# Kernel optimization log

Hardware: AMD Instinct MI355X
Metric: run time of the kernel (lower is better)

Reference implementation:

```python
import jax, jax.numpy as jnp
import numpy as np

B, L, NUM_AA, E, H = 128, 2048, 20, 16, 128

def _mlp(x, W1, b1, W2, b2, W3, b3):
    h = jax.nn.relu(x @ W1 + b1)
    h = jax.nn.relu(h @ W2 + b2)
    return h @ W3 + b3

def _mlp_params(key, in_dim):
    k1, k2, k3 = jax.random.split(key, 3)
    W1 = jax.random.normal(k1, (in_dim, H), jnp.float32) / np.sqrt(in_dim)
    W2 = jax.random.normal(k2, (H, H), jnp.float32) / np.sqrt(H)
    W3 = jax.random.normal(k3, (H, 1), jnp.float32) / np.sqrt(H)
    return W1, jnp.zeros((H,), jnp.float32), W2, jnp.zeros((H,), jnp.float32), W3, jnp.zeros((1,), jnp.float32)

def setup_inputs() -> dict:
    key = jax.random.key(0)
    kR, ks, ke, kl, kt, kp = jax.random.split(key, 6)
    inp = {
        'R': jax.random.normal(kR, (B, L, 3), jnp.float32) * 3.8,  # ~CA-CA scale
        'seq': jax.random.randint(ks, (B, L), 0, NUM_AA),
        'emb': jax.random.normal(ke, (NUM_AA, E), jnp.float32),
    }
    for pref, k, d in (('fl', kl, 1 + 2 * E), ('ft', kt, 1 + 3 * E), ('fp', kp, 2 + 4 * E)):
        W1, b1, W2, b2, W3, b3 = _mlp_params(k, d)
        inp.update({f'{pref}_W1': W1, f'{pref}_b1': b1, f'{pref}_W2': W2, f'{pref}_b2': b2, f'{pref}_W3': W3, f'{pref}_b3': b3})
    return inp

def _energy(R, e, fl, ft, fp):
    d = R[:, 1:, :] - R[:, :-1, :]                      # [B,L-1,3] bond vectors
    lengths = jnp.linalg.norm(d, axis=-1)               # [B,L-1]
    x_l = jnp.concatenate([lengths[..., None], e[:, :-1, :], e[:, 1:, :]], axis=-1)
    E_l = _mlp(x_l, *fl)[..., 0].sum(axis=1)
    # bond angles at atom i+1 between (R[i]-R[i+1]) and (R[i+2]-R[i+1])
    u, v = -d[:, :-1, :], d[:, 1:, :]                   # [B,L-2,3]
    cos_t = jnp.sum(u * v, axis=-1) / (jnp.linalg.norm(u, axis=-1) * jnp.linalg.norm(v, axis=-1))
    theta_in = jnp.clip(cos_t, -1.0, 1.0)               # use_cos_theta=True -> cos(arccos(clip))
    x_t = jnp.concatenate([theta_in[..., None], e[:, :-2, :], e[:, 1:-1, :], e[:, 2:, :]], axis=-1)
    E_t = _mlp(x_t, *ft)[..., 0].sum(axis=1)
    # torsions over quadruples
    b1, b2, b3 = d[:, :-2, :], d[:, 1:-1, :], d[:, 2:, :]
    n1 = jnp.cross(b1, b2)
    n2 = jnp.cross(b2, b3)
    b2u = b2 / jnp.linalg.norm(b2, axis=-1, keepdims=True)
    m1 = jnp.cross(n1, b2u)
    phi = jnp.arctan2(jnp.sum(m1 * n2, axis=-1), jnp.sum(n1 * n2, axis=-1))  # [B,L-3]
    sc = jnp.stack([jnp.sin(phi), jnp.cos(phi)], axis=-1)                    # [B,L-3,2]
    x_p = jnp.concatenate([sc, e[:, :-3, :], e[:, 1:-2, :], e[:, 2:-1, :], e[:, 3:, :]], axis=-1)
    E_p = _mlp(x_p, *fp)[..., 0].sum(axis=1)
    return E_l + E_t + E_p

def reference(R, seq, emb,
              fl_W1, fl_b1, fl_W2, fl_b2, fl_W3, fl_b3,
              ft_W1, ft_b1, ft_W2, ft_b2, ft_W3, ft_b3,
              fp_W1, fp_b1, fp_W2, fp_b2, fp_W3, fp_b3):
    e = emb[seq]                                        # [B,L,E]
    return _energy(R, e,
                   (fl_W1, fl_b1, fl_W2, fl_b2, fl_W3, fl_b3),
                   (ft_W1, ft_b1, ft_W2, ft_b2, ft_W3, ft_b3),
                   (fp_W1, fp_b1, fp_W2, fp_b2, fp_W3, fp_b3))
```

## Files before the change

kernel.cpp:

```cpp
#include <hip/hip_runtime.h>


typedef short bf16x8 __attribute__((ext_vector_type(8)));
typedef float f32x4  __attribute__((ext_vector_type(4)));

constexpr int Lc  = 2048;
constexpr int SHs = 136;

union FragU { uint4 u; bf16x8 v; };

__device__ __forceinline__ unsigned short f2bf(float f) {
    union { float f; unsigned u; } v; v.f = f;
    unsigned u = v.u;
    u = u + 0x7FFFu + ((u >> 16) & 1u);
    return (unsigned short)(u >> 16);
}

__device__ __forceinline__ unsigned pkbf(float a, float b) {
    unsigned ua = __float_as_uint(a) + 0x8000u;
    unsigned ub = __float_as_uint(b) + 0x8000u;
    return __builtin_amdgcn_perm(ub, ua, 0x07060302u);
}

__global__ __launch_bounds__(256)
void prep_kernel(const float* __restrict__ W1_0, const float* __restrict__ b1_0,
                 const float* __restrict__ W1_1, const float* __restrict__ b1_1,
                 const float* __restrict__ W1_2, const float* __restrict__ b1_2,
                 const float* __restrict__ W2_0, const float* __restrict__ W2_1,
                 const float* __restrict__ W2_2,
                 const float* __restrict__ emb, char* __restrict__ ws,
                 float* __restrict__ out)
{
    const int tid = blockIdx.x * 256 + threadIdx.x;
    const int np  = gridDim.x * 256;
    if (blockIdx.x == 0 && threadIdx.x < 128) out[threadIdx.x] = 0.0f;

    unsigned short* d2 = (unsigned short*)ws;
    for (int o = tid; o < 3 * 16384; o += np) {
        int t = o >> 14, r = o & 16383, col = r >> 7, k = r & 127;
        const float* W2 = (t == 0) ? W2_0 : (t == 1) ? W2_1 : W2_2;
        d2[o] = f2bf(W2[k * 128 + col]);
    }
    unsigned short* d1 = (unsigned short*)(ws + 98304);
    for (int o = tid; o < 3 * 12288; o += np) {
        int t = o / 12288, r = o - t * 12288, hid = r / 96, k = r - hid * 96;
        const int NE16 = (t == 0) ? 32 : (t == 1) ? 48 : 64;
        const int NG   = (t == 2) ? 2 : 1;
        const float* W1 = (t == 0) ? W1_0 : (t == 1) ? W1_1 : W1_2;
        const float* b1 = (t == 0) ? b1_0 : (t == 1) ? b1_1 : b1_2;
        float v = 0.0f;
        if (k >= 16) {
            int j = k - 16;
            if (j < NE16) v = W1[(NG + j) * 128 + hid];
        } else if (k == 4) v = b1[hid];
        else if (t == 0 && k == 0) v = W1_0[hid];
        else if (t == 1 && k == 1) v = W1_1[hid];
        else if (t == 2 && k == 2) v = W1_2[hid];
        else if (t == 2 && k == 3) v = W1_2[128 + hid];
        d1[o] = f2bf(v);
    }
    unsigned short* eb = (unsigned short*)(ws + 172032);
    for (int i = tid; i < 320; i += np) eb[i] = f2bf(emb[i]);
}

struct SMem {
    unsigned short H1s[64 * SHs];
    float  Rbuf[393];
    uint2  geomh[128];
    int    seqb[132];
    unsigned short ebuf[320];
    float  part[4];
};

template<int TYPE, int H>
__device__ __forceinline__ void half_pass(
    SMem& sm, const char* __restrict__ ws,
    const float* __restrict__ b2, const float* __restrict__ w3,
    int i0, int wv, int q, int c, f32x4& p4)
{
    constexpr int NEMB  = (TYPE == 0) ? 2 : (TYPE == 1) ? 3 : 4;
    constexpr int KS    = (TYPE == 2) ? 3 : 2;
    constexpr int ROWSB = Lc - 1 - TYPE;

    const unsigned short* w1t = (const unsigned short*)(ws + 98304 + TYPE * 24576);
    const unsigned short* w2t = (const unsigned short*)(ws + TYPE * 32768);

    FragU A1[2][3];
#pragma unroll
    for (int mt = 0; mt < 2; ++mt)
#pragma unroll
        for (int ks = 0; ks < KS; ++ks)
            A1[mt][ks].u = *(const uint4*)&w1t[(wv * 32 + mt * 16 + c) * 96 + ks * 32 + q * 8];

    f32x4 acc1[2][4];
#pragma unroll
    for (int mt = 0; mt < 2; ++mt)
#pragma unroll
        for (int nt = 0; nt < 4; ++nt)
            acc1[mt][nt] = (f32x4){0.f, 0.f, 0.f, 0.f};

#pragma unroll
    for (int ks = 0; ks < KS; ++ks) {
        const int k0 = ks * 32 + q * 8;
        const int j = (k0 - 16) >> 4, off = (k0 - 16) & 15;
#pragma unroll
        for (int nt = 0; nt < 4; ++nt) {
            const int m = H * 64 + nt * 16 + c;
            FragU bb;
            if (ks == 0 && q == 0) {
                uint2 g = sm.geomh[m];
                bb.u = make_uint4(g.x, g.y, 0x00003F80u, 0u);
            } else if (k0 >= 16 && j < NEMB) {
                bb.u = *(const uint4*)&sm.ebuf[sm.seqb[m + j] * 16 + off];
            } else {
                bb.u = make_uint4(0u, 0u, 0u, 0u);
            }
            acc1[0][nt] = __builtin_amdgcn_mfma_f32_16x16x32_bf16(A1[0][ks].v, bb.v, acc1[0][nt], 0, 0, 0);
            acc1[1][nt] = __builtin_amdgcn_mfma_f32_16x16x32_bf16(A1[1][ks].v, bb.v, acc1[1][nt], 0, 0, 0);
        }
    }

    const f32x4 z4 = (f32x4){0.f, 0.f, 0.f, 0.f};
#pragma unroll
    for (int mt = 0; mt < 2; ++mt)
#pragma unroll
        for (int nt = 0; nt < 4; ++nt) {
            f32x4 v = __builtin_elementwise_max(acc1[mt][nt], z4);
            uint2 pk;
            pk.x = pkbf(v[0], v[1]);
            pk.y = pkbf(v[2], v[3]);
            *(uint2*)&sm.H1s[(nt * 16 + c) * SHs + wv * 32 + mt * 16 + q * 4] = pk;
        }

    FragU B2[2][4];
#pragma unroll
    for (int nt = 0; nt < 2; ++nt)
#pragma unroll
        for (int ks = 0; ks < 4; ++ks)
            B2[nt][ks].u = *(const uint4*)&w2t[(wv * 32 + nt * 16 + c) * 128 + ks * 32 + q * 8];
    float b2v[2], w3v[2];
#pragma unroll
    for (int nt = 0; nt < 2; ++nt) {
        int col2 = wv * 32 + nt * 16 + c;
        b2v[nt] = b2[col2]; w3v[nt] = w3[col2];
    }
    __syncthreads();

    f32x4 acc2[4][2];
#pragma unroll
    for (int mt = 0; mt < 4; ++mt)
#pragma unroll
        for (int nt = 0; nt < 2; ++nt)
            acc2[mt][nt] = (f32x4){0.f, 0.f, 0.f, 0.f};
#pragma unroll
    for (int ks = 0; ks < 4; ++ks)
#pragma unroll
        for (int mt = 0; mt < 4; ++mt) {
            bf16x8 aa = *(const bf16x8*)&sm.H1s[(mt * 16 + c) * SHs + ks * 32 + q * 8];
            acc2[mt][0] = __builtin_amdgcn_mfma_f32_16x16x32_bf16(aa, B2[0][ks].v, acc2[mt][0], 0, 0, 0);
            acc2[mt][1] = __builtin_amdgcn_mfma_f32_16x16x32_bf16(aa, B2[1][ks].v, acc2[mt][1], 0, 0, 0);
        }

#pragma unroll
    for (int mt = 0; mt < 4; ++mt) {
        int mbase = H * 64 + mt * 16 + q * 4;
        if (i0 + mbase + 3 < ROWSB) {
#pragma unroll
            for (int nt = 0; nt < 2; ++nt) {
                f32x4 v = acc2[mt][nt] + b2v[nt];
                v = __builtin_elementwise_max(v, z4);
                p4 += v * w3v[nt];
            }
        } else {
#pragma unroll
            for (int rg = 0; rg < 4; ++rg)
                if (i0 + mbase + rg < ROWSB) {
                    p4[rg] += fmaxf(acc2[mt][0][rg] + b2v[0], 0.f) * w3v[0];
                    p4[rg] += fmaxf(acc2[mt][1][rg] + b2v[1], 0.f) * w3v[1];
                }
        }
    }
    __syncthreads();
}

__global__ __launch_bounds__(256, 4)
void energy_kernel(const float* __restrict__ R, const int* __restrict__ seq,
                   const char* __restrict__ ws,
                   const float* b2_0, const float* b2_1, const float* b2_2,
                   const float* w3_0, const float* w3_1, const float* w3_2,
                   const float* b3_0, const float* b3_1, const float* b3_2,
                   float* __restrict__ out)
{
    __shared__ SMem sm;
    const int tid = threadIdx.x;
    const int b   = blockIdx.y;
    const int i0  = blockIdx.x * 128;
    const int lane = tid & 63, wv = tid >> 6;
    const int q = lane >> 4, c = lane & 15;

    for (int t = tid; t < 393; t += 256) {
        int lr = t / 3, comp = t - lr * 3;
        int row = min(i0 + lr, Lc - 1);
        sm.Rbuf[t] = R[((size_t)b * Lc + row) * 3 + comp];
    }
    for (int t = tid; t < 131; t += 256)
        sm.seqb[t] = seq[b * Lc + min(i0 + t, Lc - 1)];
    {
        const uint4* se = (const uint4*)(ws + 172032);
        for (int t = tid; t < 40; t += 256) ((uint4*)sm.ebuf)[t] = se[t];
    }
    __syncthreads();

    if (tid < 128) {
        const float* p0 = &sm.Rbuf[tid * 3];
        float ax = p0[3] - p0[0], ay = p0[4] - p0[1], az = p0[5] - p0[2];
        float bx = p0[6] - p0[3], by = p0[7] - p0[4], bz = p0[8] - p0[5];
        float cx = p0[9] - p0[6], cy = p0[10] - p0[7], cz = p0[11] - p0[8];
        float na2 = ax * ax + ay * ay + az * az;
        float len = sqrtf(na2);
        float nb2 = bx * bx + by * by + bz * bz;
        float duv = -(ax * bx + ay * by + az * bz);
        float cost = fminf(fmaxf(duv / sqrtf(na2 * nb2), -1.0f), 1.0f);
        float n1x = ay * bz - az * by, n1y = az * bx - ax * bz, n1z = ax * by - ay * bx;
        float n2x = by * cz - bz * cy, n2y = bz * cx - bx * cz, n2z = bx * cy - by * cx;
        float binv = 1.0f / sqrtf(nb2);
        float ux = bx * binv, uy = by * binv, uz = bz * binv;
        float m1x = n1y * uz - n1z * uy, m1y = n1z * ux - n1x * uz, m1z = n1x * uy - n1y * ux;
        float yv = m1x * n2x + m1y * n2y + m1z * n2z;
        float xv = n1x * n2x + n1y * n2y + n1z * n2z;
        float inv = 1.0f / sqrtf(xv * xv + yv * yv);
        sm.geomh[tid] = make_uint2(pkbf(len, cost), pkbf(yv * inv, xv * inv));
    }
    __syncthreads();

    f32x4 p4 = (f32x4){0.f, 0.f, 0.f, 0.f};
    half_pass<0, 0>(sm, ws, b2_0, w3_0, i0, wv, q, c, p4);
    half_pass<0, 1>(sm, ws, b2_0, w3_0, i0, wv, q, c, p4);
    half_pass<1, 0>(sm, ws, b2_1, w3_1, i0, wv, q, c, p4);
    half_pass<1, 1>(sm, ws, b2_1, w3_1, i0, wv, q, c, p4);
    half_pass<2, 0>(sm, ws, b2_2, w3_2, i0, wv, q, c, p4);
    half_pass<2, 1>(sm, ws, b2_2, w3_2, i0, wv, q, c, p4);

    float p = p4[0] + p4[1] + p4[2] + p4[3];
#pragma unroll
    for (int off = 32; off > 0; off >>= 1)
        p += __shfl_down(p, off);
    if (lane == 0) sm.part[wv] = p;
    __syncthreads();
    if (tid == 0) {
        float tot = sm.part[0] + sm.part[1] + sm.part[2] + sm.part[3];
        tot += b3_0[0] * (float)min(Lc - 1 - i0, 128);
        tot += b3_1[0] * (float)min(Lc - 2 - i0, 128);
        tot += b3_2[0] * (float)min(Lc - 3 - i0, 128);
        atomicAdd(&out[b], tot);
    }
}

extern "C" void kernel_launch(void* const* d_in, const int* in_sizes, int n_in,
                              void* d_out, int out_size, void* d_ws, size_t ws_size,
                              hipStream_t stream) {
    const float* R   = (const float*)d_in[0];
    const int*   seq = (const int*)d_in[1];
    const float* emb = (const float*)d_in[2];
    float* out = (float*)d_out;
    char*  ws  = (char*)d_ws;

    prep_kernel<<<dim3(96), dim3(256), 0, stream>>>(
        (const float*)d_in[3],  (const float*)d_in[4],
        (const float*)d_in[9],  (const float*)d_in[10],
        (const float*)d_in[15], (const float*)d_in[16],
        (const float*)d_in[5],  (const float*)d_in[11], (const float*)d_in[17],
        emb, ws, out);

    dim3 grid(16, 128), block(256);
    energy_kernel<<<grid, block, 0, stream>>>(
        R, seq, ws,
        (const float*)d_in[6],  (const float*)d_in[12], (const float*)d_in[18],
        (const float*)d_in[7],  (const float*)d_in[13], (const float*)d_in[19],
        (const float*)d_in[8],  (const float*)d_in[14], (const float*)d_in[20],
        out);
}
```

Baseline: 165.7 us.

## Give each wave its own 32 rows to drop block-wide barriers in MLP passes

Rewrites the per-block MLP work split so each wave owns 32 sequence rows and computes all 128 hidden units for them, instead of splitting hidden columns across waves. Each wave gets a private H1 staging buffer, and the geometry features for its rows are computed by the same wave, so all the __syncthreads between layers and passes are removed. In exchange every wave now streams the full W1 and W2 weight tiles from global/L2 for every row tile, and holds more accumulators, so occupancy is lowered to 3 blocks per CU.

Result: slower. 245.2 us (+48.0%).

```diff
diff --git a/kernel.cpp b/kernel.cpp
--- a/kernel.cpp
+++ b/kernel.cpp
@@ -64,7 +64,7 @@
 }
 
 struct SMem {
-    unsigned short H1s[64 * SHs];
+    unsigned short H1s[4][32 * SHs];
     float  Rbuf[393];
     uint2  geomh[128];
     int    seqb[132];
@@ -72,8 +72,8 @@
     float  part[4];
 };
 
-template<int TYPE, int H>
-__device__ __forceinline__ void half_pass(
+template<int TYPE>
+__device__ __forceinline__ void type_pass(
     SMem& sm, const char* __restrict__ ws,
     const float* __restrict__ b2, const float* __restrict__ w3,
     int i0, int wv, int q, int c, f32x4& p4)
@@ -84,89 +84,86 @@
 
     const unsigned short* w1t = (const unsigned short*)(ws + 98304 + TYPE * 24576);
     const unsigned short* w2t = (const unsigned short*)(ws + TYPE * 32768);
-
-    FragU A1[2][3];
-#pragma unroll
-    for (int mt = 0; mt < 2; ++mt)
-#pragma unroll
-        for (int ks = 0; ks < KS; ++ks)
-            A1[mt][ks].u = *(const uint4*)&w1t[(wv * 32 + mt * 16 + c) * 96 + ks * 32 + q * 8];
-
-    f32x4 acc1[2][4];
-#pragma unroll
-    for (int mt = 0; mt < 2; ++mt)
-#pragma unroll
-        for (int nt = 0; nt < 4; ++nt)
+    unsigned short* H1w = sm.H1s[wv];
+
+    f32x4 acc1[8][2];
+#pragma unroll
+    for (int mt = 0; mt < 8; ++mt)
+#pragma unroll
+        for (int nt = 0; nt < 2; ++nt)
             acc1[mt][nt] = (f32x4){0.f, 0.f, 0.f, 0.f};
 
 #pragma unroll
     for (int ks = 0; ks < KS; ++ks) {
         const int k0 = ks * 32 + q * 8;
         const int j = (k0 - 16) >> 4, off = (k0 - 16) & 15;
-#pragma unroll
-        for (int nt = 0; nt < 4; ++nt) {
-            const int m = H * 64 + nt * 16 + c;
-            FragU bb;
+        FragU bb[2];
+#pragma unroll
+        for (int nt = 0; nt < 2; ++nt) {
+            const int m = wv * 32 + nt * 16 + c;
             if (ks == 0 && q == 0) {
                 uint2 g = sm.geomh[m];
-                bb.u = make_uint4(g.x, g.y, 0x00003F80u, 0u);
+                bb[nt].u = make_uint4(g.x, g.y, 0x00003F80u, 0u);
             } else if (k0 >= 16 && j < NEMB) {
-                bb.u = *(const uint4*)&sm.ebuf[sm.seqb[m + j] * 16 + off];
+                bb[nt].u = *(const uint4*)&sm.ebuf[sm.seqb[m + j] * 16 + off];
             } else {
-                bb.u = make_uint4(0u, 0u, 0u, 0u);
+                bb[nt].u = make_uint4(0u, 0u, 0u, 0u);
             }
-            acc1[0][nt] = __builtin_amdgcn_mfma_f32_16x16x32_bf16(A1[0][ks].v, bb.v, acc1[0][nt], 0, 0, 0);
-            acc1[1][nt] = __builtin_amdgcn_mfma_f32_16x16x32_bf16(A1[1][ks].v, bb.v, acc1[1][nt], 0, 0, 0);
+        }
+#pragma unroll
+        for (int mt = 0; mt < 8; ++mt) {
+            FragU a;
+            a.u = *(const uint4*)&w1t[(mt * 16 + c) * 96 + ks * 32 + q * 8];
+            acc1[mt][0] = __builtin_amdgcn_mfma_f32_16x16x32_bf16(a.v, bb[0].v, acc1[mt][0], 0, 0, 0);
+            acc1[mt][1] = __builtin_amdgcn_mfma_f32_16x16x32_bf16(a.v, bb[1].v, acc1[mt][1], 0, 0, 0);
         }
     }
 
     const f32x4 z4 = (f32x4){0.f, 0.f, 0.f, 0.f};
 #pragma unroll
-    for (int mt = 0; mt < 2; ++mt)
-#pragma unroll
-        for (int nt = 0; nt < 4; ++nt) {
+    for (int mt = 0; mt < 8; ++mt)
+#pragma unroll
+        for (int nt = 0; nt < 2; ++nt) {
             f32x4 v = __builtin_elementwise_max(acc1[mt][nt], z4);
             uint2 pk;
             pk.x = pkbf(v[0], v[1]);
             pk.y = pkbf(v[2], v[3]);
-            *(uint2*)&sm.H1s[(nt * 16 + c) * SHs + wv * 32 + mt * 16 + q * 4] = pk;
-        }
-
-    FragU B2[2][4];
-#pragma unroll
-    for (int nt = 0; nt < 2; ++nt)
-#pragma unroll
-        for (int ks = 0; ks < 4; ++ks)
-            B2[nt][ks].u = *(const uint4*)&w2t[(wv * 32 + nt * 16 + c) * 128 + ks * 32 + q * 8];
-    float b2v[2], w3v[2];
-#pragma unroll
-    for (int nt = 0; nt < 2; ++nt) {
-        int col2 = wv * 32 + nt * 16 + c;
+            *(uint2*)&H1w[(nt * 16 + c) * SHs + mt * 16 + q * 4] = pk;
+        }
+
+    float b2v[8], w3v[8];
+#pragma unroll
+    for (int nt = 0; nt < 8; ++nt) {
+        int col2 = nt * 16 + c;
         b2v[nt] = b2[col2]; w3v[nt] = w3[col2];
     }
-    __syncthreads();
-
-    f32x4 acc2[4][2];
-#pragma unroll
-    for (int mt = 0; mt < 4; ++mt)
-#pragma unroll
-        for (int nt = 0; nt < 2; ++nt)
+
+    f32x4 acc2[2][8];
+#pragma unroll
+    for (int mt = 0; mt < 2; ++mt)
+#pragma unroll
+        for (int nt = 0; nt < 8; ++nt)
             acc2[mt][nt] = (f32x4){0.f, 0.f, 0.f, 0.f};
-#pragma unroll
-    for (int ks = 0; ks < 4; ++ks)
-#pragma unroll
-        for (int mt = 0; mt < 4; ++mt) {
-            bf16x8 aa = *(const bf16x8*)&sm.H1s[(mt * 16 + c) * SHs + ks * 32 + q * 8];
-            acc2[mt][0] = __builtin_amdgcn_mfma_f32_16x16x32_bf16(aa, B2[0][ks].v, acc2[mt][0], 0, 0, 0);
-            acc2[mt][1] = __builtin_amdgcn_mfma_f32_16x16x32_bf16(aa, B2[1][ks].v, acc2[mt][1], 0, 0, 0);
-        }
-
-#pragma unroll
-    for (int mt = 0; mt < 4; ++mt) {
-        int mbase = H * 64 + mt * 16 + q * 4;
+
+#pragma unroll
+    for (int ks2 = 0; ks2 < 4; ++ks2) {
+        bf16x8 aa0 = *(const bf16x8*)&H1w[(0 * 16 + c) * SHs + ks2 * 32 + q * 8];
+        bf16x8 aa1 = *(const bf16x8*)&H1w[(1 * 16 + c) * SHs + ks2 * 32 + q * 8];
+#pragma unroll
+        for (int nt = 0; nt < 8; ++nt) {
+            FragU bf;
+            bf.u = *(const uint4*)&w2t[(nt * 16 + c) * 128 + ks2 * 32 + q * 8];
+            acc2[0][nt] = __builtin_amdgcn_mfma_f32_16x16x32_bf16(aa0, bf.v, acc2[0][nt], 0, 0, 0);
+            acc2[1][nt] = __builtin_amdgcn_mfma_f32_16x16x32_bf16(aa1, bf.v, acc2[1][nt], 0, 0, 0);
+        }
+    }
+
+#pragma unroll
+    for (int mt = 0; mt < 2; ++mt) {
+        int mbase = wv * 32 + mt * 16 + q * 4;
         if (i0 + mbase + 3 < ROWSB) {
 #pragma unroll
-            for (int nt = 0; nt < 2; ++nt) {
+            for (int nt = 0; nt < 8; ++nt) {
                 f32x4 v = acc2[mt][nt] + b2v[nt];
                 v = __builtin_elementwise_max(v, z4);
                 p4 += v * w3v[nt];
@@ -174,16 +171,15 @@
         } else {
 #pragma unroll
             for (int rg = 0; rg < 4; ++rg)
-                if (i0 + mbase + rg < ROWSB) {
-                    p4[rg] += fmaxf(acc2[mt][0][rg] + b2v[0], 0.f) * w3v[0];
-                    p4[rg] += fmaxf(acc2[mt][1][rg] + b2v[1], 0.f) * w3v[1];
-                }
-        }
-    }
-    __syncthreads();
-}
-
-__global__ __launch_bounds__(256, 4)
+                if (i0 + mbase + rg < ROWSB)
+#pragma unroll
+                    for (int nt = 0; nt < 8; ++nt)
+                        p4[rg] += fmaxf(acc2[mt][nt][rg] + b2v[nt], 0.f) * w3v[nt];
+        }
+    }
+}
+
+__global__ __launch_bounds__(256, 3)
 void energy_kernel(const float* __restrict__ R, const int* __restrict__ seq,
                    const char* __restrict__ ws,
                    const float* b2_0, const float* b2_1, const float* b2_2,
@@ -211,8 +207,9 @@
     }
     __syncthreads();
 
-    if (tid < 128) {
-        const float* p0 = &sm.Rbuf[tid * 3];
+    if (lane < 32) {
+        const int r = wv * 32 + lane;
+        const float* p0 = &sm.Rbuf[r * 3];
         float ax = p0[3] - p0[0], ay = p0[4] - p0[1], az = p0[5] - p0[2];
         float bx = p0[6] - p0[3], by = p0[7] - p0[4], bz = p0[8] - p0[5];
         float cx = p0[9] - p0[6], cy = p0[10] - p0[7], cz = p0[11] - p0[8];
@@ -229,17 +226,13 @@
         float yv = m1x * n2x + m1y * n2y + m1z * n2z;
         float xv = n1x * n2x + n1y * n2y + n1z * n2z;
         float inv = 1.0f / sqrtf(xv * xv + yv * yv);
-        sm.geomh[tid] = make_uint2(pkbf(len, cost), pkbf(yv * inv, xv * inv));
-    }
-    __syncthreads();
+        sm.geomh[r] = make_uint2(pkbf(len, cost), pkbf(yv * inv, xv * inv));
+    }
 
     f32x4 p4 = (f32x4){0.f, 0.f, 0.f, 0.f};
-    half_pass<0, 0>(sm, ws, b2_0, w3_0, i0, wv, q, c, p4);
-    half_pass<0, 1>(sm, ws, b2_0, w3_0, i0, wv, q, c, p4);
-    half_pass<1, 0>(sm, ws, b2_1, w3_1, i0, wv, q, c, p4);
-    half_pass<1, 1>(sm, ws, b2_1, w3_1, i0, wv, q, c, p4);
-    half_pass<2, 0>(sm, ws, b2_2, w3_2, i0, wv, q, c, p4);
-    half_pass<2, 1>(sm, ws, b2_2, w3_2, i0, wv, q, c, p4);
+    type_pass<0>(sm, ws, b2_0, w3_0, i0, wv, q, c, p4);
+    type_pass<1>(sm, ws, b2_1, w3_1, i0, wv, q, c, p4);
+    type_pass<2>(sm, ws, b2_2, w3_2, i0, wv, q, c, p4);
 
     float p = p4[0] + p4[1] + p4[2] + p4[3];
 #pragma unroll
```
